# Performance work log

Measured on AMD Instinct MI355X. Metric: run time of the kernel, lower is better.

## Reference

```python
import jax, jax.numpy as jnp
import numpy as np

H = 256
EPS = 1e-5
RBF_GAMMA = 10.0
RBF_CENTERS = jnp.asarray(np.arange(0.0, np.pi, 0.1), dtype=jnp.float32)  # 32 centers


def layer_norm(x, g, b):
    m = x.mean(-1, keepdims=True)
    v = ((x - m) ** 2).mean(-1, keepdims=True)
    return (x - m) * jax.lax.rsqrt(v + EPS) * g + b


def gin(src, dst, n_nodes, node_feat, edge_feat, w1, b1, w2, b2):
    # message = h_src + h_edge ; sum-aggregate at dst ; 2-layer MLP
    msg = node_feat[src] + edge_feat                                  # [E, H]
    agg = jax.ops.segment_sum(msg, dst, num_segments=n_nodes)        # [N, H]
    return jax.nn.relu(agg @ w1 + b1) @ w2 + b2


def graph_normal(gid, n_graphs, x):
    # divide each node feature by sqrt(#nodes in its graph)
    cnt = jax.ops.segment_sum(jnp.ones((x.shape[0],), x.dtype), gid, num_segments=n_graphs)
    return x * jax.lax.rsqrt(jnp.maximum(cnt, 1.0))[gid][:, None]


def geognn_block(src, dst, gid, n_graphs, node_hidden, edge_feat, w1, b1, w2, b2, ln_g, ln_b):
    out = gin(src, dst, node_hidden.shape[0], node_hidden, edge_feat, w1, b1, w2, b2)
    out = layer_norm(out, ln_g, ln_b)
    out = graph_normal(gid, n_graphs, out)
    # activation=False, dropout is identity in eval mode
    return out + node_hidden


def setup_inputs() -> dict:
    key = jax.random.key(0)
    ks = jax.random.split(key, 24)
    N, E, A, G = 65536, 131072, 262144, 2048
    nC = RBF_CENTERS.shape[0]
    s = 1.0 / np.sqrt(H)
    inp = {
        "node_hidden": jax.random.normal(ks[0], (N, H), jnp.float32),
        "edge_hidden": jax.random.normal(ks[1], (E, H), jnp.float32),
        "bond_angle": jax.random.uniform(ks[2], (A,), jnp.float32) * np.float32(np.pi),
        "ab_src": jax.random.randint(ks[3], (N * 2,), 0, N).astype(jnp.int64)[:E],
        "ab_dst": jax.random.randint(ks[4], (E,), 0, N).astype(jnp.int64),
        "ba_src": jax.random.randint(ks[5], (A,), 0, E).astype(jnp.int64),
        "ba_dst": jax.random.randint(ks[6], (A,), 0, E).astype(jnp.int64),
        "node_gid": jnp.sort(jax.random.randint(ks[7], (N,), 0, G)).astype(jnp.int64),
        "bond_gid": jnp.sort(jax.random.randint(ks[8], (E,), 0, G)).astype(jnp.int64),
        "num_graphs": G,
        # bond-angle RBF linear
        "rbf_w": jax.random.normal(ks[9], (nC, H), jnp.float32) / np.sqrt(nC),
        "rbf_b": jnp.zeros((H,), jnp.float32),
        # bond_angle_gnn (GIN MLP + LayerNorm)
        "ba_w1": jax.random.normal(ks[10], (H, 2 * H), jnp.float32) * s,
        "ba_b1": jnp.zeros((2 * H,), jnp.float32),
        "ba_w2": jax.random.normal(ks[11], (2 * H, H), jnp.float32) * s,
        "ba_b2": jnp.zeros((H,), jnp.float32),
        "ba_ln_g": jnp.ones((H,), jnp.float32),
        "ba_ln_b": jnp.zeros((H,), jnp.float32),
        # atom_bond_gnn
        "ab_w1": jax.random.normal(ks[12], (H, 2 * H), jnp.float32) * s,
        "ab_b1": jnp.zeros((2 * H,), jnp.float32),
        "ab_w2": jax.random.normal(ks[13], (2 * H, H), jnp.float32) * s,
        "ab_b2": jnp.zeros((H,), jnp.float32),
        "ab_ln_g": jnp.ones((H,), jnp.float32),
        "ab_ln_b": jnp.zeros((H,), jnp.float32),
    }
    return inp


def reference(node_hidden, edge_hidden, bond_angle, ab_src, ab_dst, ba_src, ba_dst,
              node_gid, bond_gid, num_graphs, rbf_w, rbf_b,
              ba_w1, ba_b1, ba_w2, ba_b2, ba_ln_g, ba_ln_b,
              ab_w1, ab_b1, ab_w2, ab_b2, ab_ln_g, ab_ln_b):
    # RBF encode bond angles -> angle edge features [A, H]
    rbf = jnp.exp(-RBF_GAMMA * (bond_angle[:, None] - RBF_CENTERS[None, :]) ** 2)
    angle_hidden = rbf @ rbf_w + rbf_b
    # bond-angle GNN updates bond features (nodes of bond_angle graph)
    edge_out = geognn_block(ba_src, ba_dst, bond_gid, num_graphs,
                            edge_hidden, angle_hidden,
                            ba_w1, ba_b1, ba_w2, ba_b2, ba_ln_g, ba_ln_b)
    # atom-bond GNN updates atom features using updated bond features as edge feats
    node_out = geognn_block(ab_src, ab_dst, node_gid, num_graphs,
                            node_hidden, edge_out,
                            ab_w1, ab_b1, ab_w2, ab_b2, ab_ln_g, ab_ln_b)
    # average pooling over atoms per graph
    cnt = jax.ops.segment_sum(jnp.ones((node_out.shape[0],), node_out.dtype), node_gid,
                              num_segments=num_graphs)
    graph_repr = jax.ops.segment_sum(node_out, node_gid, num_segments=num_graphs) / jnp.maximum(cnt, 1.0)[:, None]
    return node_out, edge_out, graph_repr
```

## Files before the change

### kernel.cpp

```cpp
#include <hip/hip_runtime.h>

#define HDIM 256
#define LNEPS 1e-5f

typedef float f32x4 __attribute__((ext_vector_type(4)));
typedef short bf16x8 __attribute__((ext_vector_type(8)));

static __device__ __forceinline__ unsigned short f2b(float f) {
  union { float f; unsigned u; } v; v.f = f;
  return (unsigned short)((v.u + 0x7fffu + ((v.u >> 16) & 1u)) >> 16);
}
static __device__ __forceinline__ unsigned pk2(float lo, float hi) {
  return (unsigned)f2b(lo) | ((unsigned)f2b(hi) << 16);
}

static __device__ __forceinline__ void gload_lds16(const void* g, void* l) {
  __builtin_amdgcn_global_load_lds((const __attribute__((address_space(1))) unsigned int*)g,
                                   (__attribute__((address_space(3))) unsigned int*)l, 16, 0, 0);
}

__global__ void pack_all_kernel(const float* __restrict__ w1a, const float* __restrict__ w2a,
                                const float* __restrict__ w1b, const float* __restrict__ w2b,
                                unsigned short* __restrict__ o1a, unsigned short* __restrict__ o2a,
                                unsigned short* __restrict__ o1b, unsigned short* __restrict__ o2b) {
  int sel = blockIdx.x >> 9;
  int o = (blockIdx.x & 511) * 256 + threadIdx.x;
  int ke = o & 7, lane = (o >> 3) & 63, tt = (o >> 9) & 1, w = (o >> 10) & 3, sl = o >> 12;
  int l15 = lane & 15, lg = lane >> 4;
  if (sel == 0 || sel == 2) {
    const float* in = (sel == 0) ? w1a : w1b;
    unsigned short* out = (sel == 0) ? o1a : o1b;
    int h = sl >> 3, kk = sl & 7;
    int n1 = h * 128 + w * 32 + tt * 16 + l15;
    int k = kk * 32 + lg * 8 + ke;
    out[o] = f2b(in[k * 512 + n1]);
  } else {
    const float* in = (sel == 1) ? w2a : w2b;
    unsigned short* out = (sel == 1) ? o2a : o2b;
    int h = sl >> 3, q = sl & 7, h2 = q >> 2, kk2 = q & 3;
    int n2 = h2 * 128 + w * 32 + tt * 16 + l15;
    int k2 = h * 128 + kk2 * 32 + lg * 8 + ke;
    out[o] = f2b(in[k2 * 256 + n2]);
  }
}

__global__ void prep_kernel(const int* __restrict__ node_gid, const int* __restrict__ bond_gid,
                            const int* __restrict__ ab_dst, const int* __restrict__ ba_dst,
                            int* cnt_node, int* cnt_bond, int* deg_n, int* deg_e,
                            int N, int E, int A) {
  int i = blockIdx.x * 256 + threadIdx.x;
  if (i < N) atomicAdd(&cnt_node[node_gid[i]], 1);
  if (i < E) {
    atomicAdd(&cnt_bond[bond_gid[i]], 1);
    atomicAdd(&deg_n[ab_dst[i]], 1);
  }
  if (i < A) atomicAdd(&deg_e[ba_dst[i]], 1);
}

__global__ void scan1_both_kernel(const int* __restrict__ degE, const int* __restrict__ degN,
                                  int* __restrict__ offE, int* __restrict__ offN,
                                  int* __restrict__ bsum, int E, int N, int nbE) {
  int b = blockIdx.x;
  const int* deg; int* excl; int* bs; int n; int bb;
  if (b < nbE) { deg = degE; excl = offE; bs = bsum; n = E; bb = b; }
  else { deg = degN; excl = offN; bs = bsum + 512; n = N; bb = b - nbE; }
  int t = threadIdx.x;
  int i = bb * 256 + t;
  int v = (i < n) ? deg[i] : 0;
  int lane = t & 63, w = t >> 6;
  int s = v;
#pragma unroll
  for (int d = 1; d < 64; d <<= 1) {
    int u = __shfl_up(s, d);
    if (lane >= d) s += u;
  }
  __shared__ int wsum[4];
  if (lane == 63) wsum[w] = s;
  __syncthreads();
  int base = 0;
  for (int ww = 0; ww < w; ++ww) base += wsum[ww];
  if (i < n) excl[i] = base + s - v;
  if (t == 255) bs[bb] = base + s;
}

__global__ void scan2_both_kernel(int* __restrict__ bsum, int nbE, int nbN) {
  int* bs = bsum + blockIdx.x * 512;
  int nb = (blockIdx.x == 0) ? nbE : nbN;
  int t = threadIdx.x;
  int v = (t < nb) ? bs[t] : 0;
  int lane = t & 63, w = t >> 6;
  int s = v;
#pragma unroll
  for (int d = 1; d < 64; d <<= 1) {
    int u = __shfl_up(s, d);
    if (lane >= d) s += u;
  }
  __shared__ int wsum[16];
  if (lane == 63) wsum[w] = s;
  __syncthreads();
  int base = 0;
  for (int ww = 0; ww < w; ++ww) base += wsum[ww];
  if (t < nb) bs[t] = base + s - v;
}

__global__ void scan3f_kernel(int* __restrict__ offE, int* __restrict__ offN,
                              const int* __restrict__ bsum,
                              const int* __restrict__ cnt_node, const int* __restrict__ cnt_bond,
                              float* fac_node, float* fac_bond, float* recip_node,
                              int E, int N, int G, int nbE, int nbN) {
  int b = blockIdx.x;
  if (b < nbE) {
    int i = b * 256 + threadIdx.x;
    if (i < E) offE[i] += bsum[b];
  } else if (b < nbE + nbN) {
    int bb = b - nbE;
    int i = bb * 256 + threadIdx.x;
    if (i < N) offN[i] += bsum[512 + bb];
  } else {
    int g = (b - nbE - nbN) * 256 + threadIdx.x;
    if (g < G) {
      float cn = fmaxf((float)cnt_node[g], 1.f);
      float cb = fmaxf((float)cnt_bond[g], 1.f);
      fac_node[g] = rsqrtf(cn);
      fac_bond[g] = rsqrtf(cb);
      recip_node[g] = 1.f / cn;
    }
  }
}

__global__ void fill_both_kernel(const int* __restrict__ ba_dst, const int* __restrict__ ab_dst,
                                 const int* __restrict__ offE, const int* __restrict__ offN,
                                 int* __restrict__ curE, int* __restrict__ curN,
                                 int* __restrict__ csrE, int* __restrict__ csrN,
                                 int A, int E, int nbA) {
  int b = blockIdx.x;
  if (b < nbA) {
    int i = b * 256 + threadIdx.x;
    if (i < A) {
      int d = ba_dst[i];
      int p = atomicAdd(&curE[d], 1);
      csrE[offE[d] + p] = i;
    }
  } else {
    int i = (b - nbA) * 256 + threadIdx.x;
    if (i < E) {
      int d = ab_dst[i];
      int p = atomicAdd(&curN[d], 1);
      csrN[offN[d] + p] = i;
    }
  }
}

__global__ __launch_bounds__(256) void angle_gather_kernel(
    const float* __restrict__ bond_angle, const int* __restrict__ ba_src,
    const float* __restrict__ edge_hidden,
    const int* __restrict__ off, const int* __restrict__ deg, const int* __restrict__ csr,
    const float* __restrict__ rbf_w, const float* __restrict__ rbf_b,
    float* __restrict__ agg_e, int E) {
  __shared__ float rbfw_s[32 * 256];
  int t = threadIdx.x;
  int w = t >> 6, lane = t & 63;
#pragma unroll
  for (int i = 0; i < 8; ++i)
    *(f32x4*)&rbfw_s[(t + i * 256) * 4] = *(const f32x4*)&rbf_w[(t + i * 256) * 4];
  __syncthreads();
  int c4 = lane * 4;
  f32x4 bv = *(const f32x4*)&rbf_b[c4];
  float cc = 0.1f * (float)(lane & 31);
  for (int rr = 0; rr < 2; ++rr) {
    int d = blockIdx.x * 8 + w * 2 + rr;
    if (d >= E) break;
    int start = off[d], cnt = deg[d];
    f32x4 acc = (f32x4)0.f;
    float rbfs = 0.f;
    for (int base = 0; base < cnt; base += 64) {
      int n = cnt - base; if (n > 64) n = 64;
      float av = 0.f;
      int s = 0;
      if (lane < n) {
        int a = csr[start + base + lane];
        av = bond_angle[a];
        s = ba_src[a];
      }
#pragma unroll 4
      for (int i = 0; i < n; ++i) {
        float avi = __shfl(av, i);
        int si = __shfl(s, i);
        if (lane < 32) {
          float dd = avi - cc;
          rbfs += __expf(-10.f * dd * dd);
        }
        acc += *(const f32x4*)&edge_hidden[(size_t)si * HDIM + c4];
      }
    }
#pragma unroll 8
    for (int k = 0; k < 32; ++k) {
      float rv = __shfl(rbfs, k);
      f32x4 wv = *(const f32x4*)&rbfw_s[k * 256 + c4];
      acc[0] += rv * wv[0]; acc[1] += rv * wv[1];
      acc[2] += rv * wv[2]; acc[3] += rv * wv[3];
    }
    float fc = (float)cnt;
    acc[0] += fc * bv[0]; acc[1] += fc * bv[1];
    acc[2] += fc * bv[2]; acc[3] += fc * bv[3];
    *(f32x4*)&agg_e[(size_t)d * HDIM + c4] = acc;
  }
}

__global__ __launch_bounds__(256) void node_gather_kernel(
    const float* __restrict__ node_hidden, const float* __restrict__ edge_out,
    const int* __restrict__ ab_src,
    const int* __restrict__ off, const int* __restrict__ deg, const int* __restrict__ csr,
    float* __restrict__ agg_n, int N) {
  int w = threadIdx.x >> 6, lane = threadIdx.x & 63;
  int d = blockIdx.x * 4 + w;
  if (d >= N) return;
  int c4 = lane * 4;
  int start = off[d], cnt = deg[d];
  f32x4 acc = (f32x4)0.f;
  for (int base = 0; base < cnt; base += 64) {
    int n = cnt - base; if (n > 64) n = 64;
    int e = 0, s = 0;
    if (lane < n) {
      e = csr[start + base + lane];
      s = ab_src[e];
    }
#pragma unroll 4
    for (int i = 0; i < n; ++i) {
      int ei = __shfl(e, i);
      int si = __shfl(s, i);
      f32x4 a = *(const f32x4*)&edge_out[(size_t)ei * HDIM + c4];
      f32x4 b = *(const f32x4*)&node_hidden[(size_t)si * HDIM + c4];
      acc += a;
      acc += b;
    }
  }
  *(f32x4*)&agg_n[(size_t)d * HDIM + c4] = acc;
}

template <int POOL>
__global__ __launch_bounds__(256, 4) void mlp_kernel(
    const float* agg_in, float* out_rows,
    const float* __restrict__ residual, const int* __restrict__ gid,
    const float* __restrict__ gfactor,
    const unsigned short* __restrict__ w1p, const float* __restrict__ b1,
    const unsigned short* __restrict__ w2p, const float* __restrict__ b2,
    const float* __restrict__ ln_g, const float* __restrict__ ln_b,
    float* pool_out, int M) {
  __shared__ __align__(16) char smem[40960];
  char* Xb = smem;
  char* Hb = smem + 16384;
  char* Wr = smem + 24576;
  char* OutsB = smem;
  float* psA = (float*)(smem + 32768);
  float* psB = (float*)(smem + 33280);
  float* fstat = (float*)(smem + 33792);
  float* gfs = (float*)(smem + 34048);
  int* gid_s = (int*)(smem + 34176);

  int t = threadIdx.x;
  int row0 = blockIdx.x * 32;
  int w = t >> 6, lane = t & 63;
  int l15 = lane & 15, lg = lane >> 4;

  char* ring = Wr + w * 4096;
  auto issue_slab = [&](int ss) {
    int hh = ss >> 4, r = ss & 15;
    const unsigned short* p = (r < 8) ? (w1p + (size_t)(hh * 8 + r) * 4096)
                                      : (w2p + (size_t)(hh * 8 + (r - 8)) * 4096);
    const char* g = (const char*)p + w * 2048 + lane * 16;
    char* dst = ring + (ss & 1) * 2048;
    gload_lds16(g, dst);
    gload_lds16(g + 1024, dst + 1024);
  };

  issue_slab(0);
  {
    int row = t >> 3;
    int c0 = (t & 7) * 32;
    int gr = row0 + row; if (gr >= M) gr = M - 1;
    const float* src = agg_in + (size_t)gr * HDIM + c0;
#pragma unroll
    for (int i = 0; i < 4; ++i) {
      f32x4 a = *(const f32x4*)(src + i * 8);
      f32x4 b = *(const f32x4*)(src + i * 8 + 4);
      int byte = (row * 512 + (c0 + i * 8) * 2) ^ ((row & 7) << 4);
      *(uint4*)(Xb + byte) =
          make_uint4(pk2(a[0], a[1]), pk2(a[2], a[3]), pk2(b[0], b[1]), pk2(b[2], b[3]));
    }
  }
  __syncthreads();

  f32x4 acc2[2][4];
#pragma unroll
  for (int mt = 0; mt < 2; ++mt)
#pragma unroll
    for (int nf = 0; nf < 4; ++nf) acc2[mt][nf] = (f32x4)0.f;

  for (int h = 0; h < 4; ++h) {
    f32x4 acc1[2][2];
#pragma unroll
    for (int tt = 0; tt < 2; ++tt)
#pragma unroll
      for (int mt = 0; mt < 2; ++mt) acc1[tt][mt] = (f32x4)0.f;

#pragma unroll
    for (int kk = 0; kk < 8; ++kk) {
      asm volatile("s_waitcnt vmcnt(0)" ::: "memory");
      const char* wbuf = ring + (kk & 1) * 2048;
      bf16x8 afr0 = *(const bf16x8*)(wbuf + lane * 16);
      bf16x8 afr1 = *(const bf16x8*)(wbuf + 1024 + lane * 16);
      bf16x8 xfr0, xfr1;
      {
        int byte0 = (l15 * 512 + kk * 64 + lg * 16) ^ ((l15 & 7) << 4);
        xfr0 = *(const bf16x8*)(Xb + byte0);
        int m = 16 + l15;
        int byte1 = (m * 512 + kk * 64 + lg * 16) ^ ((m & 7) << 4);
        xfr1 = *(const bf16x8*)(Xb + byte1);
      }
      __builtin_amdgcn_sched_barrier(0);
      issue_slab(h * 16 + kk + 1);
      acc1[0][0] = __builtin_amdgcn_mfma_f32_16x16x32_bf16(afr0, xfr0, acc1[0][0], 0, 0, 0);
      acc1[0][1] = __builtin_amdgcn_mfma_f32_16x16x32_bf16(afr0, xfr1, acc1[0][1], 0, 0, 0);
      acc1[1][0] = __builtin_amdgcn_mfma_f32_16x16x32_bf16(afr1, xfr0, acc1[1][0], 0, 0, 0);
      acc1[1][1] = __builtin_amdgcn_mfma_f32_16x16x32_bf16(afr1, xfr1, acc1[1][1], 0, 0, 0);
    }

#pragma unroll
    for (int tt = 0; tt < 2; ++tt) {
      f32x4 b1v = *(const f32x4*)&b1[h * 128 + w * 32 + tt * 16 + lg * 4];
#pragma unroll
      for (int mt = 0; mt < 2; ++mt) {
        f32x4 v = acc1[tt][mt] + b1v;
        v[0] = fmaxf(v[0], 0.f); v[1] = fmaxf(v[1], 0.f);
        v[2] = fmaxf(v[2], 0.f); v[3] = fmaxf(v[3], 0.f);
        int m = mt * 16 + l15;
        int n1l = w * 32 + tt * 16 + lg * 4;
        int byte = (m * 256 + n1l * 2) ^ ((m & 7) << 4);
        *(uint2*)(Hb + byte) = make_uint2(pk2(v[0], v[1]), pk2(v[2], v[3]));
      }
    }
    __syncthreads();

#pragma unroll
    for (int q = 0; q < 8; ++q) {
      asm volatile("s_waitcnt vmcnt(0)" ::: "memory");
      const char* wbuf = ring + (q & 1) * 2048;
      bf16x8 wfr0 = *(const bf16x8*)(wbuf + lane * 16);
      bf16x8 wfr1 = *(const bf16x8*)(wbuf + 1024 + lane * 16);
      int kk2 = q & 3, h2 = q >> 2;
      bf16x8 hfr0, hfr1;
      {
        int byte0 = (l15 * 256 + kk2 * 64 + lg * 16) ^ ((l15 & 7) << 4);
        hfr0 = *(const bf16x8*)(Hb + byte0);
        int m = 16 + l15;
        int byte1 = (m * 256 + kk2 * 64 + lg * 16) ^ ((m & 7) << 4);
        hfr1 = *(const bf16x8*)(Hb + byte1);
      }
      __builtin_amdgcn_sched_barrier(0);
      if (h < 3 || q < 7) issue_slab(h * 16 + 9 + q);
      acc2[0][h2 * 2 + 0] = __builtin_amdgcn_mfma_f32_16x16x32_bf16(hfr0, wfr0, acc2[0][h2 * 2 + 0], 0, 0, 0);
      acc2[0][h2 * 2 + 1] = __builtin_amdgcn_mfma_f32_16x16x32_bf16(hfr0, wfr1, acc2[0][h2 * 2 + 1], 0, 0, 0);
      acc2[1][h2 * 2 + 0] = __builtin_amdgcn_mfma_f32_16x16x32_bf16(hfr1, wfr0, acc2[1][h2 * 2 + 0], 0, 0, 0);
      acc2[1][h2 * 2 + 1] = __builtin_amdgcn_mfma_f32_16x16x32_bf16(hfr1, wfr1, acc2[1][h2 * 2 + 1], 0, 0, 0);
    }
    __syncthreads();
  }

  {
    float rs[2][4], rss[2][4];
#pragma unroll
    for (int mt = 0; mt < 2; ++mt)
#pragma unroll
      for (int jr = 0; jr < 4; ++jr) { rs[mt][jr] = 0.f; rss[mt][jr] = 0.f; }
#pragma unroll
    for (int nfi = 0; nfi < 4; ++nfi) {
      int col = (nfi >> 1) * 128 + w * 32 + (nfi & 1) * 16 + l15;
      float b2v = b2[col];
#pragma unroll
      for (int mt = 0; mt < 2; ++mt)
#pragma unroll
        for (int jr = 0; jr < 4; ++jr) {
          float v = acc2[mt][nfi][jr] + b2v;
          int row = mt * 16 + lg * 4 + jr;
          *(float*)(OutsB + (((row * 256 + col) * 4) ^ ((row & 7) << 4))) = v;
          rs[mt][jr] += v;
          rss[mt][jr] += v * v;
        }
    }
#pragma unroll
    for (int mt = 0; mt < 2; ++mt)
#pragma unroll
      for (int jr = 0; jr < 4; ++jr) {
        float sv = rs[mt][jr], ssv = rss[mt][jr];
        sv += __shfl_xor(sv, 1); ssv += __shfl_xor(ssv, 1);
        sv += __shfl_xor(sv, 2); ssv += __shfl_xor(ssv, 2);
        sv += __shfl_xor(sv, 4); ssv += __shfl_xor(ssv, 4);
        sv += __shfl_xor(sv, 8); ssv += __shfl_xor(ssv, 8);
        if (l15 == 0) {
          int r = mt * 16 + lg * 4 + jr;
          psA[r * 4 + w] = sv;
          psB[r * 4 + w] = ssv;
        }
      }
    if (t < 32) {
      int r = row0 + t;
      int g = (r < M) ? gid[r] : 0;
      gid_s[t] = g;
      gfs[t] = gfactor[g];
    }
  }
  __syncthreads();
  if (t < 32) {
    float sv = psA[t * 4] + psA[t * 4 + 1] + psA[t * 4 + 2] + psA[t * 4 + 3];
    float ssv = psB[t * 4] + psB[t * 4 + 1] + psB[t * 4 + 2] + psB[t * 4 + 3];
    float mean = sv * (1.f / 256.f);
    float var = ssv * (1.f / 256.f) - mean * mean;
    fstat[t * 2] = mean;
    fstat[t * 2 + 1] = rsqrtf(var + LNEPS);
  }
  __syncthreads();

  {
    float g_t = ln_g[t], bb_t = ln_b[t];
    float psum = 0.f;
    int curg = -1;
#pragma unroll 4
    for (int p = 0; p < 32; ++p) {
      int gr = row0 + p;
      if (gr < M) {
        float v = *(const float*)(OutsB + (((p * 256 + t) * 4) ^ ((p & 7) << 4)));
        v = (v - fstat[p * 2]) * fstat[p * 2 + 1] * g_t + bb_t;
        v *= gfs[p];
        v += residual[(size_t)gr * HDIM + t];
        out_rows[(size_t)gr * HDIM + t] = v;
        if (POOL) {
          int g = gid_s[p];
          if (g != curg) {
            if (curg >= 0) atomicAdd(&pool_out[(size_t)curg * HDIM + t], psum);
            psum = 0.f;
            curg = g;
          }
          psum += v;
        }
      }
    }
    if (POOL && curg >= 0) atomicAdd(&pool_out[(size_t)curg * HDIM + t], psum);
  }
}

__global__ void pooldiv_kernel(float* out_graph, const float* __restrict__ recip_node) {
  int g = blockIdx.x, t = threadIdx.x;
  out_graph[(size_t)g * HDIM + t] *= recip_node[g];
}

extern "C" void kernel_launch(void* const* d_in, const int* in_sizes, int n_in,
                              void* d_out, int out_size, void* d_ws, size_t ws_size,
                              hipStream_t stream) {
  const float* node_hidden = (const float*)d_in[0];
  const float* edge_hidden = (const float*)d_in[1];
  const float* bond_angle = (const float*)d_in[2];
  const int* ab_src = (const int*)d_in[3];
  const int* ab_dst = (const int*)d_in[4];
  const int* ba_src = (const int*)d_in[5];
  const int* ba_dst = (const int*)d_in[6];
  const int* node_gid = (const int*)d_in[7];
  const int* bond_gid = (const int*)d_in[8];
  const float* rbf_w = (const float*)d_in[10];
  const float* rbf_b = (const float*)d_in[11];
  const float* ba_w1 = (const float*)d_in[12];
  const float* ba_b1 = (const float*)d_in[13];
  const float* ba_w2 = (const float*)d_in[14];
  const float* ba_b2 = (const float*)d_in[15];
  const float* ba_ln_g = (const float*)d_in[16];
  const float* ba_ln_b = (const float*)d_in[17];
  const float* ab_w1 = (const float*)d_in[18];
  const float* ab_b1 = (const float*)d_in[19];
  const float* ab_w2 = (const float*)d_in[20];
  const float* ab_b2 = (const float*)d_in[21];
  const float* ab_ln_g = (const float*)d_in[22];
  const float* ab_ln_b = (const float*)d_in[23];

  int N = in_sizes[0] / HDIM;
  int E = in_sizes[1] / HDIM;
  int A = in_sizes[2];
  int G = out_size / HDIM - N - E;

  float* out_node = (float*)d_out;
  float* out_edge = out_node + (size_t)N * HDIM;
  float* out_graph = out_edge + (size_t)E * HDIM;

  char* ws = (char*)d_ws;
  int* cnt_node = (int*)ws;
  int* cnt_bond = cnt_node + G;
  int* deg_e = cnt_bond + G;
  int* cur_e = deg_e + E;
  int* deg_n = cur_e + E;
  int* cur_n = deg_n + N;
  size_t zero_bytes = (size_t)(2 * G + 2 * E + 2 * N) * 4;
  float* fac_node = (float*)(cur_n + N);
  float* fac_bond = fac_node + G;
  float* recip_node = fac_bond + G;
  int* off_e = (int*)(recip_node + G);
  int* csr_e = off_e + E;
  int* off_n = csr_e + A;
  int* csr_n = off_n + N;
  int* bsum = csr_n + E;
  size_t off = ((size_t)((char*)(bsum + 1024) - ws) + 255) & ~(size_t)255;
  unsigned short* w1p_ba = (unsigned short*)(ws + off); off += (size_t)512 * 256 * 2;
  unsigned short* w2p_ba = (unsigned short*)(ws + off); off += (size_t)256 * 512 * 2;
  unsigned short* w1p_ab = (unsigned short*)(ws + off); off += (size_t)512 * 256 * 2;
  unsigned short* w2p_ab = (unsigned short*)(ws + off); off += (size_t)256 * 512 * 2;

  hipMemsetAsync(d_ws, 0, zero_bytes, stream);
  hipMemsetAsync(out_graph, 0, (size_t)G * HDIM * 4, stream);

  pack_all_kernel<<<2048, 256, 0, stream>>>(ba_w1, ba_w2, ab_w1, ab_w2,
                                            w1p_ba, w2p_ba, w1p_ab, w2p_ab);

  prep_kernel<<<(A + 255) / 256, 256, 0, stream>>>(node_gid, bond_gid, ab_dst, ba_dst,
                                                   cnt_node, cnt_bond, deg_n, deg_e, N, E, A);

  int nbE = (E + 255) / 256;
  int nbN = (N + 255) / 256;
  int nbA = (A + 255) / 256;
  int nbG = (G + 255) / 256;
  scan1_both_kernel<<<nbE + nbN, 256, 0, stream>>>(deg_e, deg_n, off_e, off_n, bsum, E, N, nbE);
  scan2_both_kernel<<<2, 1024, 0, stream>>>(bsum, nbE, nbN);
  scan3f_kernel<<<nbE + nbN + nbG, 256, 0, stream>>>(off_e, off_n, bsum, cnt_node, cnt_bond,
                                                     fac_node, fac_bond, recip_node,
                                                     E, N, G, nbE, nbN);
  fill_both_kernel<<<nbA + nbE, 256, 0, stream>>>(ba_dst, ab_dst, off_e, off_n,
                                                  cur_e, cur_n, csr_e, csr_n, A, E, nbA);

  angle_gather_kernel<<<(E + 7) / 8, 256, 0, stream>>>(bond_angle, ba_src, edge_hidden,
                                                       off_e, deg_e, csr_e, rbf_w, rbf_b,
                                                       out_edge, E);
  mlp_kernel<0><<<(E + 31) / 32, 256, 0, stream>>>(out_edge, out_edge, edge_hidden, bond_gid,
                                                   fac_bond, w1p_ba, ba_b1, w2p_ba, ba_b2,
                                                   ba_ln_g, ba_ln_b, nullptr, E);

  node_gather_kernel<<<(N + 3) / 4, 256, 0, stream>>>(node_hidden, out_edge, ab_src,
                                                      off_n, deg_n, csr_n, out_node, N);
  mlp_kernel<1><<<(N + 31) / 32, 256, 0, stream>>>(out_node, out_node, node_hidden, node_gid,
                                                   fac_node, w1p_ab, ab_b1, w2p_ab, ab_b2,
                                                   ab_ln_g, ab_ln_b, out_graph, N);

  pooldiv_kernel<<<G, 256, 0, stream>>>(out_graph, recip_node);
}
```

Before: 622.0 us.

## Load MLP weight fragments directly into registers, fold pool division, widen angle blocks

The MLP kernel no longer stages bf16 weight slabs through an LDS ring with global_load_lds and vmcnt waits. Each wave now loads its fragments straight from global memory into registers, prefetching one step ahead, which cuts LDS usage and the explicit wait barriers. The per-graph mean division moves into the pooling atomics, so the separate pooldiv kernel is dropped. The angle gather kernel now handles 4 rows per wave instead of 2, halving the grid size. The trade-off is more register pressure and exposed global-load latency on the weight path.

```diff
diff --git a/kernel.cpp b/kernel.cpp
--- a/kernel.cpp
+++ b/kernel.cpp
@@ -12,11 +12,6 @@
 }
 static __device__ __forceinline__ unsigned pk2(float lo, float hi) {
   return (unsigned)f2b(lo) | ((unsigned)f2b(hi) << 16);
-}
-
-static __device__ __forceinline__ void gload_lds16(const void* g, void* l) {
-  __builtin_amdgcn_global_load_lds((const __attribute__((address_space(1))) unsigned int*)g,
-                                   (__attribute__((address_space(3))) unsigned int*)l, 16, 0, 0);
 }
 
 __global__ void pack_all_kernel(const float* __restrict__ w1a, const float* __restrict__ w2a,
@@ -167,8 +162,8 @@
   int c4 = lane * 4;
   f32x4 bv = *(const f32x4*)&rbf_b[c4];
   float cc = 0.1f * (float)(lane & 31);
-  for (int rr = 0; rr < 2; ++rr) {
-    int d = blockIdx.x * 8 + w * 2 + rr;
+  for (int rr = 0; rr < 4; ++rr) {
+    int d = blockIdx.x * 16 + w * 4 + rr;
     if (d >= E) break;
     int start = off[d], cnt = deg[d];
     f32x4 acc = (f32x4)0.f;
@@ -242,39 +237,36 @@
 __global__ __launch_bounds__(256, 4) void mlp_kernel(
     const float* agg_in, float* out_rows,
     const float* __restrict__ residual, const int* __restrict__ gid,
-    const float* __restrict__ gfactor,
+    const float* __restrict__ gfactor, const float* __restrict__ grecip,
     const unsigned short* __restrict__ w1p, const float* __restrict__ b1,
     const unsigned short* __restrict__ w2p, const float* __restrict__ b2,
     const float* __restrict__ ln_g, const float* __restrict__ ln_b,
     float* pool_out, int M) {
-  __shared__ __align__(16) char smem[40960];
+  __shared__ __align__(16) char smem[34432];
   char* Xb = smem;
   char* Hb = smem + 16384;
-  char* Wr = smem + 24576;
   char* OutsB = smem;
   float* psA = (float*)(smem + 32768);
   float* psB = (float*)(smem + 33280);
   float* fstat = (float*)(smem + 33792);
   float* gfs = (float*)(smem + 34048);
-  int* gid_s = (int*)(smem + 34176);
+  float* grs = (float*)(smem + 34176);
+  int* gid_s = (int*)(smem + 34304);
 
   int t = threadIdx.x;
   int row0 = blockIdx.x * 32;
   int w = t >> 6, lane = t & 63;
   int l15 = lane & 15, lg = lane >> 4;
 
-  char* ring = Wr + w * 4096;
-  auto issue_slab = [&](int ss) {
-    int hh = ss >> 4, r = ss & 15;
-    const unsigned short* p = (r < 8) ? (w1p + (size_t)(hh * 8 + r) * 4096)
-                                      : (w2p + (size_t)(hh * 8 + (r - 8)) * 4096);
-    const char* g = (const char*)p + w * 2048 + lane * 16;
-    char* dst = ring + (ss & 1) * 2048;
-    gload_lds16(g, dst);
-    gload_lds16(g + 1024, dst + 1024);
-  };
-
-  issue_slab(0);
+  const unsigned short* w1f = w1p + ((size_t)(w * 2) * 64 + lane) * 8;
+  const unsigned short* w2f = w2p + ((size_t)(w * 2) * 64 + lane) * 8;
+#define W1F(hh, kk, tt) (*(const bf16x8*)(w1f + (size_t)((hh) * 8 + (kk)) * 4096 + (tt) * 512))
+#define W2F(hh, q, nf) (*(const bf16x8*)(w2f + (size_t)((hh) * 8 + (q)) * 4096 + (nf) * 512))
+
+  bf16x8 wcur0, wcur1, wnxt0, wnxt1;
+  wcur0 = W1F(0, 0, 0);
+  wcur1 = W1F(0, 0, 1);
+
   {
     int row = t >> 3;
     int c0 = (t & 7) * 32;
@@ -306,10 +298,13 @@
 
 #pragma unroll
     for (int kk = 0; kk < 8; ++kk) {
-      asm volatile("s_waitcnt vmcnt(0)" ::: "memory");
-      const char* wbuf = ring + (kk & 1) * 2048;
-      bf16x8 afr0 = *(const bf16x8*)(wbuf + lane * 16);
-      bf16x8 afr1 = *(const bf16x8*)(wbuf + 1024 + lane * 16);
+      if (kk < 7) {
+        wnxt0 = W1F(h, kk + 1, 0);
+        wnxt1 = W1F(h, kk + 1, 1);
+      } else {
+        wnxt0 = W2F(h, 0, 0);
+        wnxt1 = W2F(h, 0, 1);
+      }
       bf16x8 xfr0, xfr1;
       {
         int byte0 = (l15 * 512 + kk * 64 + lg * 16) ^ ((l15 & 7) << 4);
@@ -318,12 +313,12 @@
         int byte1 = (m * 512 + kk * 64 + lg * 16) ^ ((m & 7) << 4);
         xfr1 = *(const bf16x8*)(Xb + byte1);
       }
-      __builtin_amdgcn_sched_barrier(0);
-      issue_slab(h * 16 + kk + 1);
-      acc1[0][0] = __builtin_amdgcn_mfma_f32_16x16x32_bf16(afr0, xfr0, acc1[0][0], 0, 0, 0);
-      acc1[0][1] = __builtin_amdgcn_mfma_f32_16x16x32_bf16(afr0, xfr1, acc1[0][1], 0, 0, 0);
-      acc1[1][0] = __builtin_amdgcn_mfma_f32_16x16x32_bf16(afr1, xfr0, acc1[1][0], 0, 0, 0);
-      acc1[1][1] = __builtin_amdgcn_mfma_f32_16x16x32_bf16(afr1, xfr1, acc1[1][1], 0, 0, 0);
+      acc1[0][0] = __builtin_amdgcn_mfma_f32_16x16x32_bf16(wcur0, xfr0, acc1[0][0], 0, 0, 0);
+      acc1[0][1] = __builtin_amdgcn_mfma_f32_16x16x32_bf16(wcur0, xfr1, acc1[0][1], 0, 0, 0);
+      acc1[1][0] = __builtin_amdgcn_mfma_f32_16x16x32_bf16(wcur1, xfr0, acc1[1][0], 0, 0, 0);
+      acc1[1][1] = __builtin_amdgcn_mfma_f32_16x16x32_bf16(wcur1, xfr1, acc1[1][1], 0, 0, 0);
+      wcur0 = wnxt0;
+      wcur1 = wnxt1;
     }
 
 #pragma unroll
@@ -344,10 +339,13 @@
 
 #pragma unroll
     for (int q = 0; q < 8; ++q) {
-      asm volatile("s_waitcnt vmcnt(0)" ::: "memory");
-      const char* wbuf = ring + (q & 1) * 2048;
-      bf16x8 wfr0 = *(const bf16x8*)(wbuf + lane * 16);
-      bf16x8 wfr1 = *(const bf16x8*)(wbuf + 1024 + lane * 16);
+      if (q < 7) {
+        wnxt0 = W2F(h, q + 1, 0);
+        wnxt1 = W2F(h, q + 1, 1);
+      } else if (h < 3) {
+        wnxt0 = W1F(h + 1, 0, 0);
+        wnxt1 = W1F(h + 1, 0, 1);
+      }
       int kk2 = q & 3, h2 = q >> 2;
       bf16x8 hfr0, hfr1;
       {
@@ -357,15 +355,17 @@
         int byte1 = (m * 256 + kk2 * 64 + lg * 16) ^ ((m & 7) << 4);
         hfr1 = *(const bf16x8*)(Hb + byte1);
       }
-      __builtin_amdgcn_sched_barrier(0);
-      if (h < 3 || q < 7) issue_slab(h * 16 + 9 + q);
-      acc2[0][h2 * 2 + 0] = __builtin_amdgcn_mfma_f32_16x16x32_bf16(hfr0, wfr0, acc2[0][h2 * 2 + 0], 0, 0, 0);
-      acc2[0][h2 * 2 + 1] = __builtin_amdgcn_mfma_f32_16x16x32_bf16(hfr0, wfr1, acc2[0][h2 * 2 + 1], 0, 0, 0);
-      acc2[1][h2 * 2 + 0] = __builtin_amdgcn_mfma_f32_16x16x32_bf16(hfr1, wfr0, acc2[1][h2 * 2 + 0], 0, 0, 0);
-      acc2[1][h2 * 2 + 1] = __builtin_amdgcn_mfma_f32_16x16x32_bf16(hfr1, wfr1, acc2[1][h2 * 2 + 1], 0, 0, 0);
+      acc2[0][h2 * 2 + 0] = __builtin_amdgcn_mfma_f32_16x16x32_bf16(hfr0, wcur0, acc2[0][h2 * 2 + 0], 0, 0, 0);
+      acc2[0][h2 * 2 + 1] = __builtin_amdgcn_mfma_f32_16x16x32_bf16(hfr0, wcur1, acc2[0][h2 * 2 + 1], 0, 0, 0);
+      acc2[1][h2 * 2 + 0] = __builtin_amdgcn_mfma_f32_16x16x32_bf16(hfr1, wcur0, acc2[1][h2 * 2 + 0], 0, 0, 0);
+      acc2[1][h2 * 2 + 1] = __builtin_amdgcn_mfma_f32_16x16x32_bf16(hfr1, wcur1, acc2[1][h2 * 2 + 1], 0, 0, 0);
+      wcur0 = wnxt0;
+      wcur1 = wnxt1;
     }
     __syncthreads();
   }
+#undef W1F
+#undef W2F
 
   {
     float rs[2][4], rss[2][4];
@@ -408,6 +408,7 @@
       int g = (r < M) ? gid[r] : 0;
       gid_s[t] = g;
       gfs[t] = gfactor[g];
+      if (POOL) grs[t] = grecip[g];
     }
   }
   __syncthreads();
@@ -424,6 +425,7 @@
   {
     float g_t = ln_g[t], bb_t = ln_b[t];
     float psum = 0.f;
+    float currecip = 0.f;
     int curg = -1;
 #pragma unroll 4
     for (int p = 0; p < 32; ++p) {
@@ -437,21 +439,17 @@
         if (POOL) {
           int g = gid_s[p];
           if (g != curg) {
-            if (curg >= 0) atomicAdd(&pool_out[(size_t)curg * HDIM + t], psum);
+            if (curg >= 0) atomicAdd(&pool_out[(size_t)curg * HDIM + t], psum * currecip);
             psum = 0.f;
             curg = g;
+            currecip = grs[p];
           }
           psum += v;
         }
       }
     }
-    if (POOL && curg >= 0) atomicAdd(&pool_out[(size_t)curg * HDIM + t], psum);
-  }
-}
-
-__global__ void pooldiv_kernel(float* out_graph, const float* __restrict__ recip_node) {
-  int g = blockIdx.x, t = threadIdx.x;
-  out_graph[(size_t)g * HDIM + t] *= recip_node[g];
+    if (POOL && curg >= 0) atomicAdd(&pool_out[(size_t)curg * HDIM + t], psum * currecip);
+  }
 }
 
 extern "C" void kernel_launch(void* const* d_in, const int* in_sizes, int n_in,
@@ -533,18 +531,16 @@
   fill_both_kernel<<<nbA + nbE, 256, 0, stream>>>(ba_dst, ab_dst, off_e, off_n,
                                                   cur_e, cur_n, csr_e, csr_n, A, E, nbA);
 
-  angle_gather_kernel<<<(E + 7) / 8, 256, 0, stream>>>(bond_angle, ba_src, edge_hidden,
-                                                       off_e, deg_e, csr_e, rbf_w, rbf_b,
-                                                       out_edge, E);
+  angle_gather_kernel<<<(E + 15) / 16, 256, 0, stream>>>(bond_angle, ba_src, edge_hidden,
+                                                         off_e, deg_e, csr_e, rbf_w, rbf_b,
+                                                         out_edge, E);
   mlp_kernel<0><<<(E + 31) / 32, 256, 0, stream>>>(out_edge, out_edge, edge_hidden, bond_gid,
-                                                   fac_bond, w1p_ba, ba_b1, w2p_ba, ba_b2,
-                                                   ba_ln_g, ba_ln_b, nullptr, E);
+                                                   fac_bond, nullptr, w1p_ba, ba_b1, w2p_ba,
+                                                   ba_b2, ba_ln_g, ba_ln_b, nullptr, E);
 
   node_gather_kernel<<<(N + 3) / 4, 256, 0, stream>>>(node_hidden, out_edge, ab_src,
                                                       off_n, deg_n, csr_n, out_node, N);
   mlp_kernel<1><<<(N + 31) / 32, 256, 0, stream>>>(out_node, out_node, node_hidden, node_gid,
-                                                   fac_node, w1p_ab, ab_b1, w2p_ab, ab_b2,
-                                                   ab_ln_g, ab_ln_b, out_graph, N);
-
-  pooldiv_kernel<<<G, 256, 0, stream>>>(out_graph, recip_node);
-}
+                                                   fac_node, recip_node, w1p_ab, ab_b1, w2p_ab,
+                                                   ab_b2, ab_ln_g, ab_ln_b, out_graph, N);
+}
```

Result: faster. 567.7 us (-8.7%).
